# Kernel optimization log

Measured on AMD Instinct MI355X. Metric: run time of the kernel, lower is better.

The kernel has to match this reference:

```python
import jax, jax.numpy as jnp
import numpy as np

B, N, D = 8, 8192, 512
H, WIDTH = 8, 2048
DH = D // H
EPS = 1e-5


def _ln(x, g, b):
    m = jnp.mean(x, axis=-1, keepdims=True)
    v = jnp.mean(jnp.square(x - m), axis=-1, keepdims=True)
    return (x - m) * jax.lax.rsqrt(v + EPS) * g + b


def setup_inputs() -> dict:
    key = jax.random.key(0)
    ks = jax.random.split(key, 16)
    s = 0.02
    return {
        "x": jax.random.normal(ks[0], (B, N, D), dtype=jnp.float32),
        "mask": jnp.ones((B, N), dtype=jnp.float32),
        "Wq": jax.random.normal(ks[1], (D, D), dtype=jnp.float32) * s,
        "bq": jnp.zeros((D,), dtype=jnp.float32),
        "Wk": jax.random.normal(ks[2], (D, D), dtype=jnp.float32) * s,
        "bk": jnp.zeros((D,), dtype=jnp.float32),
        "Wv": jax.random.normal(ks[3], (D, D), dtype=jnp.float32) * s,
        "bv": jnp.zeros((D,), dtype=jnp.float32),
        "q_alpha": jax.random.normal(ks[4], (H, DH), dtype=jnp.float32),
        "k_beta": jax.random.normal(ks[5], (H, DH), dtype=jnp.float32),
        "Wo": jax.random.normal(ks[6], (D, D), dtype=jnp.float32) * s,
        "bo": jnp.zeros((D,), dtype=jnp.float32),
        "ln0_g": jnp.ones((D,), dtype=jnp.float32),
        "ln0_b": jnp.zeros((D,), dtype=jnp.float32),
        "ln1_g": jnp.ones((D,), dtype=jnp.float32),
        "ln1_b": jnp.zeros((D,), dtype=jnp.float32),
        "W1": jax.random.normal(ks[7], (WIDTH, D), dtype=jnp.float32) * s,
        "b1": jnp.zeros((WIDTH,), dtype=jnp.float32),
        "W2": jax.random.normal(ks[8], (D, WIDTH), dtype=jnp.float32) * s,
        "b2": jnp.zeros((D,), dtype=jnp.float32),
    }


def reference(x, mask, Wq, bq, Wk, bk, Wv, bv, q_alpha, k_beta, Wo, bo,
              ln0_g, ln0_b, ln1_g, ln1_b, W1, b1, W2, b2):
    scale = DH ** -0.5
    mask_ = mask[..., None]                       # [B,N,1]
    valid = (mask != 0)[..., None]                # [B,N,1] bool, broadcast over H

    residual = x
    xn = _ln(x, ln0_g, ln0_b) * mask_

    Q = (xn @ Wq.T + bq).reshape(B, N, H, DH)
    K = (xn @ Wk.T + bk).reshape(B, N, H, DH)
    V = (xn @ Wv.T + bv).reshape(B, N, H, DH)

    # stage 1: global query pooling
    alpha = jnp.einsum('bnhd,hd->bnh', Q, q_alpha) * scale
    alpha = jnp.where(valid, alpha, -jnp.inf)
    alpha = jax.nn.softmax(alpha, axis=1)         # softmax over N
    global_q = jnp.einsum('bnhd,bnh->bhd', Q, alpha)

    # stage 2: global value pooling
    P = K * global_q[:, None]                     # [B,N,H,DH]
    beta = jnp.einsum('bnhd,hd->bnh', P, k_beta) * scale
    beta = jnp.where(valid, beta, -jnp.inf)
    beta = jax.nn.softmax(beta, axis=1)
    global_v = jnp.einsum('bnhd,bnh->bhd', V, beta)

    out = (Q + global_v[:, None]).reshape(B, N, D)
    out = out @ Wo.T + bo
    x = residual + out

    residual = x
    xn = _ln(x, ln1_g, ln1_b)
    h = jax.nn.gelu(xn @ W1.T + b1, approximate=False)
    h = jax.nn.gelu(h @ W2.T + b2, approximate=False)
    x = residual + h
    x = x * mask_
    return x
```

## Files before the change

### kernel.cpp

```cpp
#include <hip/hip_runtime.h>
#include <hip/hip_bf16.h>
#include <math.h>

typedef short s8v __attribute__((ext_vector_type(8)));
typedef short s4v __attribute__((ext_vector_type(4)));
typedef __bf16 bf8v __attribute__((ext_vector_type(8)));
typedef float f4v __attribute__((ext_vector_type(4)));

#define GLOBAL_AS __attribute__((address_space(1)))
#define LDS_AS __attribute__((address_space(3)))

static __device__ __forceinline__ float bf2f(ushort u) {
  return __builtin_bit_cast(float, (unsigned int)u << 16);
}
static __device__ __forceinline__ ushort f2bf(float f) {
  unsigned int u = __builtin_bit_cast(unsigned int, f);
  u += 0x7FFFu + ((u >> 16) & 1u);
  return (ushort)(u >> 16);
}
static __device__ __forceinline__ float gelu_f(float v) {
  float t = v * v;
  float u = v * (0.0356774081f * t + 0.7978845608f);
  float e = __expf(-2.0f * u);
  return v * __builtin_amdgcn_rcpf(1.0f + e);
}
static __device__ __forceinline__ float wave_max_f(float v) {
  #pragma unroll
  for (int o = 32; o >= 1; o >>= 1) v = fmaxf(v, __shfl_xor(v, o));
  return v;
}
static __device__ __forceinline__ float wave_sum_f(float v) {
  #pragma unroll
  for (int o = 32; o >= 1; o >>= 1) v += __shfl_xor(v, o);
  return v;
}
static __device__ __forceinline__ void gload16(const ushort* g, const ushort* l) {
  __builtin_amdgcn_global_load_lds(
      (const GLOBAL_AS unsigned int*)g,
      (LDS_AS unsigned int*)l, 16, 0, 0);
}

__global__ void cvt_f32_bf16(const float* __restrict__ in, ushort* __restrict__ out, int n) {
  int i = (blockIdx.x * 256 + threadIdx.x) * 4;
  if (i >= n) return;
  float4 v = *(const float4*)(in + i);
  s4v o;
  o[0] = (short)f2bf(v.x); o[1] = (short)f2bf(v.y);
  o[2] = (short)f2bf(v.z); o[3] = (short)f2bf(v.w);
  *(s4v*)(out + i) = o;
}

__global__ __launch_bounds__(256) void transpose512(
    const float* __restrict__ in, float* __restrict__ out) {
  __shared__ float t[32][33];
  const int bx = blockIdx.x & 15, by = blockIdx.x >> 4;
  const int tx = threadIdx.x & 31, ty = threadIdx.x >> 5;
  #pragma unroll
  for (int i = 0; i < 4; ++i)
    t[ty + i * 8][tx] = in[(long)(by * 32 + ty + i * 8) * 512 + bx * 32 + tx];
  __syncthreads();
  #pragma unroll
  for (int i = 0; i < 4; ++i)
    out[(long)(bx * 32 + ty + i * 8) * 512 + by * 32 + tx] = t[tx][ty + i * 8];
}

__global__ __launch_bounds__(256) void wqo_kernel(
    const float* __restrict__ Wo, const float* __restrict__ Wq,
    ushort* __restrict__ WqoB)
{
  __shared__ float lO[64][33];
  __shared__ float lQ[32][65];
  const int t = threadIdx.x;
  const int bi = (blockIdx.x & 7) * 64, bj = (blockIdx.x >> 3) * 64;
  float acc[16] = {};
  for (int k0 = 0; k0 < 512; k0 += 32) {
    __syncthreads();
    {
      const int r = t >> 2, c = (t & 3) * 8;
      #pragma unroll
      for (int j = 0; j < 8; ++j) lO[r][c + j] = Wo[(long)(bi + r) * 512 + k0 + c + j];
      const int r2 = t >> 3, c2 = (t & 7) * 8;
      #pragma unroll
      for (int j = 0; j < 8; ++j) lQ[r2][c2 + j] = Wq[(long)(k0 + r2) * 512 + bj + c2 + j];
    }
    __syncthreads();
    const int j = t & 63, ig = t >> 6;
    for (int kk = 0; kk < 32; ++kk) {
      float q = lQ[kk][j];
      #pragma unroll
      for (int ii = 0; ii < 16; ++ii) acc[ii] += lO[ig * 16 + ii][kk] * q;
    }
  }
  const int j = t & 63, ig = t >> 6;
  #pragma unroll
  for (int ii = 0; ii < 16; ++ii)
    WqoB[(long)(bi + ig * 16 + ii) * 512 + bj + j] = f2bf(acc[ii]);
}

__global__ __launch_bounds__(256) void wa_kernel(
    const float* __restrict__ qa, const float* __restrict__ Wq,
    const float* __restrict__ bqv, ushort* __restrict__ waB, float* __restrict__ ca)
{
  __shared__ float ql[64];
  const int h = blockIdx.x;
  const int t = threadIdx.x;
  if (h >= 8) {
    waB[h * 512 + t] = 0; waB[h * 512 + 256 + t] = 0;
    if (t == 0) ca[h] = 0.f;
    return;
  }
  if (t < 64) ql[t] = qa[h * 64 + t];
  __syncthreads();
  #pragma unroll
  for (int half = 0; half < 2; ++half) {
    const int k = half * 256 + t;
    float s = 0;
    for (int dd = 0; dd < 64; ++dd) s += ql[dd] * Wq[(long)(h * 64 + dd) * 512 + k];
    waB[h * 512 + k] = f2bf(s);
  }
  if (t == 0) {
    float s = 0;
    for (int dd = 0; dd < 64; ++dd) s += ql[dd] * bqv[h * 64 + dd];
    ca[h] = s;
  }
}

__global__ __launch_bounds__(256) void ln_rows(
    const float* __restrict__ x, const float* __restrict__ gam,
    const float* __restrict__ bet, const float* __restrict__ mask,
    ushort* __restrict__ out)
{
  const int tid = threadIdx.x, lane = tid & 63, wv = tid >> 6;
  const long row = (long)blockIdx.x * 4 + wv;
  const float* xp = x + row * 512 + lane * 8;
  float4 a = *(const float4*)xp;
  float4 b = *(const float4*)(xp + 4);
  float s = a.x + a.y + a.z + a.w + b.x + b.y + b.z + b.w;
  float q = a.x*a.x + a.y*a.y + a.z*a.z + a.w*a.w
          + b.x*b.x + b.y*b.y + b.z*b.z + b.w*b.w;
  s = wave_sum_f(s); q = wave_sum_f(q);
  float m = s * (1.f / 512.f);
  float var = q * (1.f / 512.f) - m * m;
  float r = rsqrtf(var + 1e-5f);
  float mk = mask ? mask[row] : 1.f;
  const float* gp = gam + lane * 8;
  const float* bp = bet + lane * 8;
  float4 g0 = *(const float4*)gp, g1 = *(const float4*)(gp + 4);
  float4 c0 = *(const float4*)bp, c1 = *(const float4*)(bp + 4);
  s8v o;
  o[0] = (short)f2bf(((a.x - m) * r * g0.x + c0.x) * mk);
  o[1] = (short)f2bf(((a.y - m) * r * g0.y + c0.y) * mk);
  o[2] = (short)f2bf(((a.z - m) * r * g0.z + c0.z) * mk);
  o[3] = (short)f2bf(((a.w - m) * r * g0.w + c0.w) * mk);
  o[4] = (short)f2bf(((b.x - m) * r * g1.x + c1.x) * mk);
  o[5] = (short)f2bf(((b.y - m) * r * g1.y + c1.y) * mk);
  o[6] = (short)f2bf(((b.z - m) * r * g1.z + c1.z) * mk);
  o[7] = (short)f2bf(((b.w - m) * r * g1.w + c1.w) * mk);
  *(s8v*)(out + row * 512 + lane * 8) = o;
}

__global__ __launch_bounds__(256) void ln_rows_bf16(
    const ushort* __restrict__ x, const float* __restrict__ gam,
    const float* __restrict__ bet, ushort* __restrict__ out)
{
  const int tid = threadIdx.x, lane = tid & 63, wv = tid >> 6;
  const long row = (long)blockIdx.x * 4 + wv;
  s8v v = *(const s8v*)(x + row * 512 + lane * 8);
  float xv[8];
  #pragma unroll
  for (int j = 0; j < 8; ++j) xv[j] = bf2f((ushort)v[j]);
  float s = 0.f, q = 0.f;
  #pragma unroll
  for (int j = 0; j < 8; ++j) { s += xv[j]; q += xv[j] * xv[j]; }
  s = wave_sum_f(s); q = wave_sum_f(q);
  float m = s * (1.f / 512.f);
  float var = q * (1.f / 512.f) - m * m;
  float r = rsqrtf(var + 1e-5f);
  const float* gp = gam + lane * 8;
  const float* bp = bet + lane * 8;
  float4 g0 = *(const float4*)gp, g1 = *(const float4*)(gp + 4);
  float4 c0 = *(const float4*)bp, c1 = *(const float4*)(bp + 4);
  float gg[8] = {g0.x, g0.y, g0.z, g0.w, g1.x, g1.y, g1.z, g1.w};
  float cc[8] = {c0.x, c0.y, c0.z, c0.w, c1.x, c1.y, c1.z, c1.w};
  s8v o;
  #pragma unroll
  for (int j = 0; j < 8; ++j) o[j] = (short)f2bf((xv[j] - m) * r * gg[j] + cc[j]);
  *(s8v*)(out + row * 512 + lane * 8) = o;
}

template<int BS, int CS>
__global__ __launch_bounds__(256) void logits_k(
    const ushort* __restrict__ XN, const ushort* __restrict__ Wl,
    const float* __restrict__ cvec, const float* __restrict__ mask,
    float* __restrict__ outL)
{
  __shared__ ushort lw[16 * 512];
  const int tid = threadIdx.x, lane = tid & 63, wv = tid >> 6;
  const long r0 = (long)blockIdx.x * 64;
  const int b = (int)(r0 >> 13);
  #pragma unroll
  for (int i = 0; i < 4; ++i) {
    const int u = tid + i * 256;
    const int h2 = u >> 6, uu = u & 63;
    s8v v = *(const s8v*)(Wl + (long)b * BS + h2 * 512 + uu * 8);
    *(s8v*)(lw + h2 * 512 + (uu ^ (h2 & 7)) * 8) = v;
  }
  __syncthreads();
  const int h = lane & 15, q = lane >> 4;
  const long rw = r0 + wv * 16;
  const ushort* ap = XN + (rw + (lane & 15)) * 512 + q * 8;
  f4v acc = {};
  #pragma unroll
  for (int t = 0; t < 16; ++t) {
    bf8v a = *(const bf8v*)(ap + t * 32);
    bf8v bb = *(const bf8v*)(lw + h * 512 + (((t * 4 + q) ^ (h & 7))) * 8);
    acc = __builtin_amdgcn_mfma_f32_16x16x32_bf16(a, bb, acc, 0, 0, 0);
  }
  const float cv = cvec[b * CS + h];
  #pragma unroll
  for (int j = 0; j < 4; ++j) {
    const long n = rw + q * 4 + j;
    float v = (acc[j] + cv) * 0.125f;
    if (mask[n] == 0.f) v = -1e30f;
    if (h < 8) outL[((long)((b << 3) + h) << 13) + (n & 8191)] = v;
  }
}

__global__ __launch_bounds__(1024) void softmax_rows(float* __restrict__ L)
{
  __shared__ float red[16];
  __shared__ float bc;
  const int tid = threadIdx.x, lane = tid & 63, wv = tid >> 6;
  float* p = L + ((long)blockIdx.x << 13) + tid * 8;
  float4 v0 = *(float4*)p;
  float4 v1 = *(float4*)(p + 4);
  float m = fmaxf(fmaxf(fmaxf(v0.x, v0.y), fmaxf(v0.z, v0.w)),
                  fmaxf(fmaxf(v1.x, v1.y), fmaxf(v1.z, v1.w)));
  m = wave_max_f(m);
  if (lane == 0) red[wv] = m;
  __syncthreads();
  if (tid < 64) {
    float t = (lane < 16) ? red[lane] : -INFINITY;
    t = wave_max_f(t);
    if (lane == 0) bc = t;
  }
  __syncthreads();
  const float gm = bc;
  v0.x = __expf(v0.x - gm); v0.y = __expf(v0.y - gm);
  v0.z = __expf(v0.z - gm); v0.w = __expf(v0.w - gm);
  v1.x = __expf(v1.x - gm); v1.y = __expf(v1.y - gm);
  v1.z = __expf(v1.z - gm); v1.w = __expf(v1.w - gm);
  float s = v0.x + v0.y + v0.z + v0.w + v1.x + v1.y + v1.z + v1.w;
  s = wave_sum_f(s);
  __syncthreads();
  if (lane == 0) red[wv] = s;
  __syncthreads();
  if (tid < 64) {
    float t = (lane < 16) ? red[lane] : 0.f;
    t = wave_sum_f(t);
    if (lane == 0) bc = t;
  }
  __syncthreads();
  const float inv = 1.0f / bc;
  v0.x *= inv; v0.y *= inv; v0.z *= inv; v0.w *= inv;
  v1.x *= inv; v1.y *= inv; v1.z *= inv; v1.w *= inv;
  *(float4*)p = v0;
  *(float4*)(p + 4) = v1;
}

__global__ __launch_bounds__(256) void pool_w(
    const ushort* __restrict__ XN, const float* __restrict__ wbuf,
    float* __restrict__ part)
{
  __shared__ float wlds[128][8];
  __shared__ float cmb[4][512];
  const int tid = threadIdx.x;
  const int b = blockIdx.x >> 6, ch = blockIdx.x & 63;
  const long g0 = ((long)b << 13) + ch * 128;
  if (tid < 128) {
    #pragma unroll
    for (int h = 0; h < 8; ++h)
      wlds[tid][h] = wbuf[(((long)(b * 8 + h)) << 13) + ch * 128 + tid];
  }
  __syncthreads();
  const int rg = tid >> 6, c8 = (tid & 63) * 8;
  f4v acc[8][2] = {};
  for (int it = 0; it < 32; ++it) {
    const int r = it * 4 + rg;
    s8v xv = *(const s8v*)(XN + (g0 + r) * 512 + c8);
    float xf[8];
    #pragma unroll
    for (int j = 0; j < 8; ++j) xf[j] = bf2f((ushort)xv[j]);
    #pragma unroll
    for (int h = 0; h < 8; ++h) {
      const float w = wlds[r][h];
      #pragma unroll
      for (int j = 0; j < 8; ++j) acc[h][j >> 2][j & 3] += w * xf[j];
    }
  }
  #pragma unroll
  for (int h = 0; h < 8; ++h) {
    __syncthreads();
    #pragma unroll
    for (int j = 0; j < 8; ++j) cmb[rg][c8 + j] = acc[h][j >> 2][j & 3];
    __syncthreads();
    const int col = tid * 2;
    float s0 = cmb[0][col] + cmb[1][col] + cmb[2][col] + cmb[3][col];
    float s1 = cmb[0][col + 1] + cmb[1][col + 1] + cmb[2][col + 1] + cmb[3][col + 1];
    *(float2*)(part + (((long)blockIdx.x * 8 + h) << 9) + col) = make_float2(s0, s1);
  }
}

__global__ __launch_bounds__(256) void combine_px(
    const float* __restrict__ part, float* __restrict__ px)
{
  const int bh = blockIdx.x;
  const int b = bh >> 3, h = bh & 7;
  const int col = threadIdx.x * 2;
  float s0 = 0.f, s1 = 0.f;
  for (int ch = 0; ch < 64; ++ch) {
    const float* p = part + (((long)((b * 64 + ch) * 8 + h)) << 9) + col;
    s0 += p[0]; s1 += p[1];
  }
  px[(bh << 9) + col] = s0;
  px[(bh << 9) + col + 1] = s1;
}

__global__ __launch_bounds__(64) void prep_gq_wb(
    const float* __restrict__ px, const float* __restrict__ WqT,
    const float* __restrict__ bqv, const float* __restrict__ kbv,
    const float* __restrict__ Wk, const float* __restrict__ bkv,
    ushort* __restrict__ wbB, float* __restrict__ cbs)
{
  __shared__ float pxl[512];
  __shared__ float gkb[64];
  const int bh = blockIdx.x, b = bh >> 3, h = bh & 7, d = threadIdx.x;
  #pragma unroll
  for (int i = 0; i < 8; ++i) pxl[d + i * 64] = px[(bh << 9) + d + i * 64];
  __syncthreads();
  float acc = bqv[h * 64 + d];
  for (int c = 0; c < 512; ++c) acc += pxl[c] * WqT[(long)c * 512 + h * 64 + d];
  gkb[d] = acc * kbv[h * 64 + d];
  __syncthreads();
  float s[8] = {};
  for (int dd = 0; dd < 64; ++dd) {
    const float g = gkb[dd];
    const float* wr = Wk + (long)(h * 64 + dd) * 512 + d;
    #pragma unroll
    for (int ki = 0; ki < 8; ++ki) s[ki] += g * wr[ki * 64];
  }
  #pragma unroll
  for (int ki = 0; ki < 8; ++ki)
    wbB[(long)(b * 16 + h) * 512 + d + ki * 64] = f2bf(s[ki]);
  if (d == 0) {
    float t = 0.f;
    for (int dd = 0; dd < 64; ++dd) t += gkb[dd] * bkv[h * 64 + dd];
    cbs[b * 16 + h] = t;
  }
  if (h == 0) {
    #pragma unroll
    for (int hp = 8; hp < 16; ++hp)
      for (int k = d; k < 512; k += 64) wbB[(long)(b * 16 + hp) * 512 + k] = 0;
    if (d < 8) cbs[b * 16 + 8 + d] = 0.f;
  }
}

__global__ __launch_bounds__(64) void prep_gv(
    const float* __restrict__ pv, const float* __restrict__ WvT,
    const float* __restrict__ bvv, const float* __restrict__ bqv,
    float* __restrict__ gvb)
{
  __shared__ float pxl[512];
  const int bh = blockIdx.x, b = bh >> 3, h = bh & 7, d = threadIdx.x;
  #pragma unroll
  for (int i = 0; i < 8; ++i) pxl[d + i * 64] = pv[(bh << 9) + d + i * 64];
  __syncthreads();
  float acc = bvv[h * 64 + d] + bqv[h * 64 + d];
  for (int c = 0; c < 512; ++c) acc += pxl[c] * WvT[(long)c * 512 + h * 64 + d];
  gvb[b * 512 + h * 64 + d] = acc;
}

__global__ __launch_bounds__(256) void bias_gv(
    const float* __restrict__ gv, const float* __restrict__ Wo,
    const float* __restrict__ bo, float* __restrict__ bo2) {
  const int b = blockIdx.x;
  const int n = blockIdx.y * 256 + threadIdx.x;
  const float* g = gv + b * 512;
  const float* w = Wo + (long)n * 512;
  float acc = 0.f;
  for (int d = 0; d < 512; d += 4) {
    float4 wv4 = *(const float4*)(w + d);
    acc += g[d] * wv4.x + g[d + 1] * wv4.y + g[d + 2] * wv4.z + g[d + 3] * wv4.w;
  }
  bo2[b * 512 + n] = bo[n] + acc;
}

#define MFMA_(d,a,b) d = __builtin_amdgcn_mfma_f32_16x16x32_bf16(a, b, d, 0, 0, 0)

template<int EPI, int LDA, int NN, int KK>
__global__ __launch_bounds__(512, 4) void gemmP(
    const ushort* __restrict__ A, const ushort* __restrict__ W,
    const float* __restrict__ bias, const void* __restrict__ resid,
    const float* __restrict__ mask, void* __restrict__ Out)
{
  constexpr int NBX = NN / 256;
  constexpr int NT = KK / 32;
  __shared__ __align__(16) ushort lds[2][12288];
  const int tid = threadIdx.x;
  const int lane = tid & 63;
  const int w = tid >> 6;
  const int wm = w >> 2, wn = w & 3;

  const int nwg = gridDim.x;
  const int cpx = nwg >> 3;
  const int wg = (blockIdx.x & 7) * cpx + (blockIdx.x >> 3);
  const int bx = wg % NBX, by = wg / NBX;
  const long bm = (long)by * 128;
  const int bn = bx * 256;

  const int scr = tid >> 2, sls = tid & 3;
  const int akU = ((sls ^ (scr & 3) ^ ((scr >> 2) & 3))) * 8;
  const ushort* asrc = A + (bm + scr) * (long)LDA + akU;
  const int rbe = (scr & 31) + ((scr >> 5) << 6);
  const ushort* besrc = W + (long)(bn + rbe) * KK + akU;
  const ushort* bosrc = W + (long)(bn + rbe + 32) * KK + akU;

#define STG_A(nb_, Tt)  gload16(asrc + (Tt) * 32, &lds[nb_][tid * 8])
#define STG_BE(nb_, Tt) gload16(besrc + (Tt) * 32, &lds[nb_][4096 + tid * 8])
#define STG_BO(nb_, Tt) gload16(bosrc + (Tt) * 32, &lds[nb_][8192 + tid * 8])

  STG_A(0, 0); STG_BE(0, 0); STG_BO(0, 0);

  f4v acc[4][4] = {};

  const int L = lane & 15, q = lane >> 4;
  const int soff = (q ^ (lane & 3) ^ ((lane >> 2) & 3)) * 8;
  const int abase = (wm * 64 + L) * 32 + soff;
  const int bbase = 4096 + (wn * 32 + L) * 32 + soff;

  asm volatile("s_waitcnt vmcnt(1)" ::: "memory");
  asm volatile("s_barrier" ::: "memory");

  for (int T = 0; T < NT; ++T) {
    const int buf = T & 1, nb = buf ^ 1;
    const ushort* Lp = &lds[buf][0];
    const bool st = (T + 1 < NT);
    bf8v aR[4], bR[4];
    #pragma unroll
    for (int m = 0; m < 4; ++m) aR[m] = *(const bf8v*)(Lp + abase + m * 512);
    bR[0] = *(const bf8v*)(Lp + bbase);
    bR[1] = *(const bf8v*)(Lp + bbase + 512);
    if (st) {
      STG_A(nb, T + 1); STG_BE(nb, T + 1);
      asm volatile("s_waitcnt vmcnt(2)" ::: "memory");
    } else {
      asm volatile("s_waitcnt vmcnt(0)" ::: "memory");
    }
    asm volatile("s_barrier" ::: "memory");
    __builtin_amdgcn_s_setprio(1);
    #pragma unroll
    for (int m = 0; m < 4; ++m) {
      MFMA_(acc[m][0], aR[m], bR[0]);
      MFMA_(acc[m][1], aR[m], bR[1]);
    }
    __builtin_amdgcn_s_setprio(0);
    bR[2] = *(const bf8v*)(Lp + bbase + 4096);
    bR[3] = *(const bf8v*)(Lp + bbase + 4096 + 512);
    if (st) {
      STG_BO(nb, T + 1);
      asm volatile("s_waitcnt vmcnt(1)" ::: "memory");
    }
    asm volatile("s_barrier" ::: "memory");
    __builtin_amdgcn_s_setprio(1);
    #pragma unroll
    for (int m = 0; m < 4; ++m) {
      MFMA_(acc[m][2], aR[m], bR[2]);
      MFMA_(acc[m][3], aR[m], bR[3]);
    }
    __builtin_amdgcn_s_setprio(0);
  }
#undef STG_A
#undef STG_BE
#undef STG_BO

  const int colb = bn + wn * 64 + L;
  const long rowb = bm + wm * 64 + q * 4;
  const float* biasp = (EPI == 5) ? bias + ((bm >> 13) << 9) : bias;
  #pragma unroll
  for (int m = 0; m < 4; ++m) {
    #pragma unroll
    for (int j = 0; j < 4; ++j) {
      const long row = rowb + m * 16 + j;
      #pragma unroll
      for (int n = 0; n < 4; ++n) {
        const int col = colb + n * 16;
        float v = acc[m][n][j] + biasp[col];
        const long idx = row * (long)NN + col;
        if constexpr (EPI == 2) {
          ((ushort*)Out)[idx] = f2bf(gelu_f(v));
        } else if constexpr (EPI == 3) {
          ((float*)Out)[idx] = (bf2f(((const ushort*)resid)[idx]) + gelu_f(v)) * mask[row];
        } else {
          ((ushort*)Out)[idx] = f2bf(v + ((const float*)resid)[idx]);
        }
      }
    }
  }
}

extern "C" void kernel_launch(void* const* d_in, const int* in_sizes, int n_in,
                              void* d_out, int out_size, void* d_ws, size_t ws_size,
                              hipStream_t stream) {
  const float* x    = (const float*)d_in[0];
  const float* mask = (const float*)d_in[1];
  const float* Wq   = (const float*)d_in[2];
  const float* bq   = (const float*)d_in[3];
  const float* Wk   = (const float*)d_in[4];
  const float* bk   = (const float*)d_in[5];
  const float* Wv   = (const float*)d_in[6];
  const float* bv   = (const float*)d_in[7];
  const float* qa   = (const float*)d_in[8];
  const float* kb   = (const float*)d_in[9];
  const float* Wo   = (const float*)d_in[10];
  const float* bo   = (const float*)d_in[11];
  const float* g0   = (const float*)d_in[12];
  const float* be0  = (const float*)d_in[13];
  const float* g1   = (const float*)d_in[14];
  const float* be1  = (const float*)d_in[15];
  const float* W1   = (const float*)d_in[16];
  const float* b1   = (const float*)d_in[17];
  const float* W2   = (const float*)d_in[18];
  const float* b2   = (const float*)d_in[19];
  float* out = (float*)d_out;

  const int M = 65536;
  char* ws = (char*)d_ws;
  const size_t MB = 1024 * 1024;
  ushort* XN  = (ushort*)(ws);
  ushort* X1  = (ushort*)(ws + 64 * MB);
  ushort* H1  = (ushort*)(ws + 192 * MB);
  float*  AL  = (float*)(ws + 192 * MB);
  float*  BL  = (float*)(ws + 194 * MB);
  float*  PART= (float*)(ws + 196 * MB);
  char* base = ws + 448 * MB;
  ushort* W1B  = (ushort*)(base);
  ushort* W2B  = (ushort*)(base + 2 * MB);
  ushort* WqoB = (ushort*)(base + 4 * MB);
  float*  WqT  = (float*)(base + 4 * MB + 512 * 1024);
  float*  WvT  = (float*)(base + 5 * MB + 512 * 1024);
  ushort* waB  = (ushort*)(base + 6 * MB + 512 * 1024);
  ushort* wbB  = (ushort*)(base + 6 * MB + 528 * 1024);
  float*  ca   = (float*)(base + 6 * MB + 656 * 1024);
  float*  cbs  = (float*)(base + 6 * MB + 660 * 1024);
  float*  PX   = (float*)(base + 6 * MB + 664 * 1024);
  float*  PV   = (float*)(base + 6 * MB + 792 * 1024);
  float*  GVB  = (float*)(base + 6 * MB + 920 * 1024);
  float*  BO2  = (float*)(base + 6 * MB + 936 * 1024);

  cvt_f32_bf16<<<1024, 256, 0, stream>>>(W1, W1B, 1048576);
  cvt_f32_bf16<<<1024, 256, 0, stream>>>(W2, W2B, 1048576);
  wqo_kernel<<<64, 256, 0, stream>>>(Wo, Wq, WqoB);
  wa_kernel<<<16, 256, 0, stream>>>(qa, Wq, bq, waB, ca);
  transpose512<<<256, 256, 0, stream>>>(Wq, WqT);
  transpose512<<<256, 256, 0, stream>>>(Wv, WvT);

  ln_rows<<<M / 4, 256, 0, stream>>>(x, g0, be0, mask, XN);

  logits_k<0, 0><<<1024, 256, 0, stream>>>(XN, waB, ca, mask, AL);
  softmax_rows<<<64, 1024, 0, stream>>>(AL);
  pool_w<<<512, 256, 0, stream>>>(XN, AL, PART);
  combine_px<<<64, 256, 0, stream>>>(PART, PX);
  prep_gq_wb<<<64, 64, 0, stream>>>(PX, WqT, bq, kb, Wk, bk, wbB, cbs);

  logits_k<8192, 16><<<1024, 256, 0, stream>>>(XN, wbB, cbs, mask, BL);
  softmax_rows<<<64, 1024, 0, stream>>>(BL);
  pool_w<<<512, 256, 0, stream>>>(XN, BL, PART);
  combine_px<<<64, 256, 0, stream>>>(PART, PV);
  prep_gv<<<64, 64, 0, stream>>>(PV, WvT, bv, bq, GVB);
  bias_gv<<<dim3(8, 2), 256, 0, stream>>>(GVB, Wo, bo, BO2);

  gemmP<5, 512, 512, 512><<<2 * (M / 128), 512, 0, stream>>>(
      XN, WqoB, BO2, x, nullptr, X1);

  ln_rows_bf16<<<M / 4, 256, 0, stream>>>(X1, g1, be1, XN);

  gemmP<2, 512, 2048, 512><<<8 * (M / 128), 512, 0, stream>>>(
      XN, W1B, b1, nullptr, nullptr, H1);
  gemmP<3, 2048, 512, 2048><<<2 * (M / 128), 512, 0, stream>>>(
      H1, W2B, b2, X1, mask, out);
}
```

Measured before the change: 712.2 us.

## Triple-buffer GEMM LDS staging with two-tile prefetch and one barrier per step

Moves the GEMM main loop from double-buffered LDS with split half-tile loads to a triple buffer that prefetches tile T+2 while computing tile T. Each iteration now has a single barrier and issues all 16 MFMAs in one block. The aim is to hide more global-load latency and halve barrier overhead. In exchange, LDS use grows to 72KB per block, which can reduce how many workgroups fit per CU against the launch bound of 4.

```diff
diff --git a/kernel.cpp b/kernel.cpp
--- a/kernel.cpp
+++ b/kernel.cpp
@@ -405,7 +405,7 @@
 {
   constexpr int NBX = NN / 256;
   constexpr int NT = KK / 32;
-  __shared__ __align__(16) ushort lds[2][12288];
+  __shared__ __align__(16) ushort lds[3][12288];
   const int tid = threadIdx.x;
   const int lane = tid & 63;
   const int w = tid >> 6;
@@ -425,11 +425,13 @@
   const ushort* besrc = W + (long)(bn + rbe) * KK + akU;
   const ushort* bosrc = W + (long)(bn + rbe + 32) * KK + akU;
 
-#define STG_A(nb_, Tt)  gload16(asrc + (Tt) * 32, &lds[nb_][tid * 8])
-#define STG_BE(nb_, Tt) gload16(besrc + (Tt) * 32, &lds[nb_][4096 + tid * 8])
-#define STG_BO(nb_, Tt) gload16(bosrc + (Tt) * 32, &lds[nb_][8192 + tid * 8])
-
-  STG_A(0, 0); STG_BE(0, 0); STG_BO(0, 0);
+#define STG(b_, Tt) { \
+    gload16(asrc + (Tt) * 32, &lds[b_][tid * 8]); \
+    gload16(besrc + (Tt) * 32, &lds[b_][4096 + tid * 8]); \
+    gload16(bosrc + (Tt) * 32, &lds[b_][8192 + tid * 8]); }
+
+  STG(0, 0);
+  STG(1, 1);
 
   f4v acc[4][4] = {};
 
@@ -438,50 +440,34 @@
   const int abase = (wm * 64 + L) * 32 + soff;
   const int bbase = 4096 + (wn * 32 + L) * 32 + soff;
 
-  asm volatile("s_waitcnt vmcnt(1)" ::: "memory");
+  asm volatile("s_waitcnt vmcnt(3)" ::: "memory");
   asm volatile("s_barrier" ::: "memory");
 
   for (int T = 0; T < NT; ++T) {
-    const int buf = T & 1, nb = buf ^ 1;
-    const ushort* Lp = &lds[buf][0];
-    const bool st = (T + 1 < NT);
+    const ushort* Lp = &lds[T % 3][0];
     bf8v aR[4], bR[4];
     #pragma unroll
     for (int m = 0; m < 4; ++m) aR[m] = *(const bf8v*)(Lp + abase + m * 512);
     bR[0] = *(const bf8v*)(Lp + bbase);
     bR[1] = *(const bf8v*)(Lp + bbase + 512);
-    if (st) {
-      STG_A(nb, T + 1); STG_BE(nb, T + 1);
-      asm volatile("s_waitcnt vmcnt(2)" ::: "memory");
+    bR[2] = *(const bf8v*)(Lp + bbase + 4096);
+    bR[3] = *(const bf8v*)(Lp + bbase + 4096 + 512);
+    if (T + 2 < NT) {
+      STG((T + 2) % 3, T + 2);
+      asm volatile("s_waitcnt vmcnt(3)" ::: "memory");
     } else {
       asm volatile("s_waitcnt vmcnt(0)" ::: "memory");
     }
     asm volatile("s_barrier" ::: "memory");
     __builtin_amdgcn_s_setprio(1);
     #pragma unroll
-    for (int m = 0; m < 4; ++m) {
-      MFMA_(acc[m][0], aR[m], bR[0]);
-      MFMA_(acc[m][1], aR[m], bR[1]);
-    }
+    for (int m = 0; m < 4; ++m)
+      #pragma unroll
+      for (int n = 0; n < 4; ++n)
+        MFMA_(acc[m][n], aR[m], bR[n]);
     __builtin_amdgcn_s_setprio(0);
-    bR[2] = *(const bf8v*)(Lp + bbase + 4096);
-    bR[3] = *(const bf8v*)(Lp + bbase + 4096 + 512);
-    if (st) {
-      STG_BO(nb, T + 1);
-      asm volatile("s_waitcnt vmcnt(1)" ::: "memory");
-    }
-    asm volatile("s_barrier" ::: "memory");
-    __builtin_amdgcn_s_setprio(1);
-    #pragma unroll
-    for (int m = 0; m < 4; ++m) {
-      MFMA_(acc[m][2], aR[m], bR[2]);
-      MFMA_(acc[m][3], aR[m], bR[3]);
-    }
-    __builtin_amdgcn_s_setprio(0);
-  }
-#undef STG_A
-#undef STG_BE
-#undef STG_BO
+  }
+#undef STG
 
   const int colb = bn + wn * 64 + L;
   const long rowb = bm + wm * 64 + q * 4;
```

Result: no change. 712.9 us (+0.1%).
